# Kernel tuning notes

Measured on AMD Instinct MI355X. Metric: run time of the kernel, lower is better.

## Reference

```python
import jax, jax.numpy as jnp
import numpy as np

T = 1.0  # temperature from __init__ (t=1)


def setup_inputs() -> dict:
    key = jax.random.key(0)
    k1, k2, k3 = jax.random.split(key, 3)
    N, C, D = 262144, 1024, 128
    feats = jax.random.normal(k1, (N, D), dtype=jnp.float32)
    prototypes = jax.random.normal(k2, (C, D), dtype=jnp.float32)
    labels = jax.random.randint(k3, (N,), 0, C, dtype=jnp.int64)
    return {"feats": feats, "prototypes": prototypes, "labels": labels}


def _dce_loss(feats, prototypes, labels):
    # same math as sqrt(sum((x[:,None,:]-y)**2, -1)) without the NxCxD tensor.
    x_sq = jnp.sum(feats * feats, axis=-1, keepdims=True)          # [N,1]
    y_sq = jnp.sum(prototypes * prototypes, axis=-1)               # [C]
    xy = jnp.einsum('nd,cd->nc', feats, prototypes)                # [N,C]
    sq_dist = jnp.maximum(x_sq + y_sq[None, :] - 2.0 * xy, 0.0)
    logits = -jnp.sqrt(sq_dist) / T                                # [N,C]
    logp = jax.nn.log_softmax(logits, axis=-1)
    nll = -jnp.take_along_axis(logp, labels[:, None], axis=-1)[:, 0]
    return jnp.mean(nll)  # CrossEntropyLoss default reduction='mean'


def reference(feats, prototypes, labels):
    return _dce_loss(feats, prototypes, labels)
```

## Files before the change

kernel.cpp:

```cpp
#include <hip/hip_runtime.h>
#include <hip/hip_bf16.h>

typedef __bf16 bf16x8 __attribute__((ext_vector_type(8)));
typedef __bf16 bf16x2 __attribute__((ext_vector_type(2)));
typedef float f32x4 __attribute__((ext_vector_type(4)));

#define LN2f 0.6931471805599453f
#define CEf  2.0402785445f
#define EXPA (-CEf * 8388608.0f)
#define EXPB ((127.0f - 0.0437f) * 8388608.0f)

typedef __attribute__((address_space(3))) unsigned int lds_u32;
typedef __attribute__((address_space(1))) unsigned int glb_u32;

__device__ __forceinline__ void gload16(const void* g, void* l) {
    __builtin_amdgcn_global_load_lds((const glb_u32*)g, (lds_u32*)l, 16, 0, 0);
}

__global__ void dce_prep(const float* __restrict__ protos,
                         unsigned short* __restrict__ bpf,
                         float* __restrict__ ysqn) {
    int c = blockIdx.x;
    int lane = threadIdx.x;
    float2 f = ((const float2*)(protos))[c * 64 + lane];
    int d0 = lane * 2;
    int kk = d0 >> 5, sub = d0 & 31, lg = sub >> 3, e = sub & 7;
    size_t o = (((size_t)((c >> 4) * 4 + kk) * 64) + lg * 16 + (c & 15)) * 8 + e;
    bf16x2 h;
    h.x = (__bf16)f.x;
    h.y = (__bf16)f.y;
    *(bf16x2*)(bpf + o) = h;
    float xs = f.x * f.x + f.y * f.y;
#pragma unroll
    for (int d = 1; d < 64; d <<= 1) xs += __shfl_xor(xs, d);
    if (lane == 0) ysqn[c] = -0.5f * xs;
}

__global__ __launch_bounds__(256, 4) void dce_main(
    const float* __restrict__ feats,
    const float* __restrict__ protos,
    const unsigned short* __restrict__ bpf,
    const float* __restrict__ ysqn,
    const int* __restrict__ labels,
    float* __restrict__ partials, int C) {
    const int tid = threadIdx.x;
    const int lane = tid & 63;
    const int w = tid >> 6;
    const int row0 = blockIdx.x * 128;
    const int rbase = row0 + w * 32;
    const int lr = lane & 15;
    const int lg = lane >> 4;

    __shared__ __align__(16) unsigned char bsm0[16384];
    __shared__ __align__(16) unsigned char bsm1[16384];
    __shared__ float red[4];

    const char* bpc = (const char*)bpf;
    const int c0 = (blockIdx.x >> 3) & 15;

#define STAGE(buf, chunkIdx)                                                   \
    {                                                                          \
        const char* src_ = bpc + (size_t)(chunkIdx) * 16384 + tid * 16;        \
        _Pragma("unroll") for (int kt = 0; kt < 4; ++kt)                       \
            gload16(src_ + kt * 4096, (buf) + kt * 4096 + tid * 16);           \
    }

    STAGE(bsm0, c0);

    const int r1 = row0 + (tid >> 1);
    const int half = tid & 1;
    const int lab = labels[r1];
    const float4* fx = (const float4*)feats + (size_t)r1 * 32 + half * 16;
    const float4* px = (const float4*)protos + (size_t)lab * 32 + half * 16;
    float xx = 0.f, yy = 0.f, xy = 0.f;
#pragma unroll
    for (int i = 0; i < 16; ++i) {
        float4 f = fx[i], p = px[i];
        xx = fmaf(f.x, f.x, fmaf(f.y, f.y, fmaf(f.z, f.z, fmaf(f.w, f.w, xx))));
        yy = fmaf(p.x, p.x, fmaf(p.y, p.y, fmaf(p.z, p.z, fmaf(p.w, p.w, yy))));
        xy = fmaf(f.x, p.x, fmaf(f.y, p.y, fmaf(f.z, p.z, fmaf(f.w, p.w, xy))));
    }
    xx += __shfl_xor(xx, 1);
    yy += __shfl_xor(yy, 1);
    xy += __shfl_xor(xy, 1);
    const float ld = __builtin_amdgcn_sqrtf(fmaxf(fmaf(-2.f, xy, xx + yy), 0.f));

    bf16x8 a[2][4];
    const float4* f4 = (const float4*)feats;
#pragma unroll
    for (int m = 0; m < 2; ++m) {
        size_t r = (size_t)(rbase + m * 16 + lr);
#pragma unroll
        for (int kk = 0; kk < 4; ++kk) {
            size_t idx = r * 32 + kk * 8 + lg * 2;
            float4 lo = f4[idx];
            float4 hi = f4[idx + 1];
            bf16x8 v;
            v[0] = (__bf16)lo.x; v[1] = (__bf16)lo.y; v[2] = (__bf16)lo.z; v[3] = (__bf16)lo.w;
            v[4] = (__bf16)hi.x; v[5] = (__bf16)hi.y; v[6] = (__bf16)hi.z; v[7] = (__bf16)hi.w;
            a[m][kk] = v;
        }
    }

    float pre[2][4];
#pragma unroll
    for (int m = 0; m < 2; ++m)
#pragma unroll
        for (int reg = 0; reg < 4; ++reg)
            pre[m][reg] = -0.5f * __shfl(xx, 2 * (m * 16 + lg * 4 + reg));

    float lacc[2][4];
#pragma unroll
    for (int m = 0; m < 2; ++m)
#pragma unroll
        for (int reg = 0; reg < 4; ++reg) lacc[m][reg] = 0.f;

    const float* ysp = ysqn + lr;

#define TILE(buf, kt, tt)                                                       \
    {                                                                           \
        const bf16x8* bl_ = (const bf16x8*)((buf) + (kt) * 4096);               \
        bf16x8 b0 = bl_[lane];                                                  \
        bf16x8 b1 = bl_[64 + lane];                                             \
        bf16x8 b2 = bl_[128 + lane];                                            \
        bf16x8 b3 = bl_[192 + lane];                                            \
        const float yq_ = ysp[(tt) * 16];                                       \
        _Pragma("unroll") for (int m = 0; m < 2; ++m) {                         \
            f32x4 acc;                                                          \
            acc[0] = pre[m][0] + yq_;                                           \
            acc[1] = pre[m][1] + yq_;                                           \
            acc[2] = pre[m][2] + yq_;                                           \
            acc[3] = pre[m][3] + yq_;                                           \
            acc = __builtin_amdgcn_mfma_f32_16x16x32_bf16(a[m][0], b0, acc, 0, 0, 0); \
            acc = __builtin_amdgcn_mfma_f32_16x16x32_bf16(a[m][1], b1, acc, 0, 0, 0); \
            acc = __builtin_amdgcn_mfma_f32_16x16x32_bf16(a[m][2], b2, acc, 0, 0, 0); \
            acc = __builtin_amdgcn_mfma_f32_16x16x32_bf16(a[m][3], b3, acc, 0, 0, 0); \
            _Pragma("unroll") for (int reg = 0; reg < 4; ++reg) {               \
                float s_ = __builtin_amdgcn_sqrtf(-acc[reg]);  \
                int i_ = (int)fmaf(s_, EXPA, EXPB);            \
                lacc[m][reg] += __int_as_float(i_);                             \
            }                                                                   \
        }                                                                       \
    }

    __syncthreads();
#pragma unroll 2
    for (int ch = 0; ch < 16; ++ch) {
        unsigned char* curb = (ch & 1) ? bsm1 : bsm0;
        unsigned char* nxtb = (ch & 1) ? bsm0 : bsm1;
        const int ci = (c0 + ch) & 15;
        if (ch + 1 < 16) {
            const int ni = (c0 + ch + 1) & 15;
            STAGE(nxtb, ni);
        }
#pragma unroll
        for (int kt = 0; kt < 4; ++kt) TILE(curb, kt, ci * 4 + kt);
        __syncthreads();
    }

#undef STAGE
#undef TILE

    float ssum = 0.f;
#pragma unroll
    for (int m = 0; m < 2; ++m)
#pragma unroll
        for (int reg = 0; reg < 4; ++reg) {
            float l = lacc[m][reg];
            l += __shfl_xor(l, 1);
            l += __shfl_xor(l, 2);
            l += __shfl_xor(l, 4);
            l += __shfl_xor(l, 8);
            float ldv = __shfl(ld, 2 * (m * 16 + lg * 4 + reg));
            if (lr == 0) ssum += ldv + LN2f * __builtin_amdgcn_logf(l);
        }
    ssum += __shfl_xor(ssum, 16);
    ssum += __shfl_xor(ssum, 32);

    if (lane == 0) red[w] = ssum;
    __syncthreads();
    if (tid == 0) partials[blockIdx.x] = red[0] + red[1] + red[2] + red[3];
}

__global__ void dce_finish(const float* __restrict__ partials,
                           float* __restrict__ out, int nblocks, float invN) {
    int tid = threadIdx.x;
    float s = 0.f;
    for (int i = tid; i < nblocks; i += 256) s += partials[i];
#pragma unroll
    for (int d = 1; d < 64; d <<= 1) s += __shfl_xor(s, d);
    __shared__ float red[4];
    if ((tid & 63) == 0) red[tid >> 6] = s;
    __syncthreads();
    if (tid == 0) out[0] = (red[0] + red[1] + red[2] + red[3]) * invN;
}

extern "C" void kernel_launch(void* const* d_in, const int* in_sizes, int n_in,
                              void* d_out, int out_size, void* d_ws, size_t ws_size,
                              hipStream_t stream) {
    const float* feats = (const float*)d_in[0];
    const float* protos = (const float*)d_in[1];
    const int* labels = (const int*)d_in[2];
    const int N = in_sizes[2];
    const int C = in_sizes[1] / 128;
    float* out = (float*)d_out;

    unsigned short* bpf = (unsigned short*)d_ws;
    float* ysqn = (float*)((char*)d_ws + (size_t)C * 128 * 2);
    float* partials = ysqn + C;
    const int nblocks = N / 128;

    dce_prep<<<C, 64, 0, stream>>>(protos, bpf, ysqn);
    dce_main<<<nblocks, 256, 0, stream>>>(feats, protos, bpf, ysqn, labels, partials, C);
    dce_finish<<<1, 256, 0, stream>>>(partials, out, nblocks, 1.0f / (float)N);
}
```

Baseline: 130.4 us.

## Triple-buffer prototype tiles with partial vmcnt waits and stage ysq in LDS

Replaces the double-buffered LDS pipeline with a three-slot ring that prefetches two chunks ahead. It waits only on older loads (vmcnt(4)) before each barrier, so the next transfer stays in flight during compute. It also copies the per-prototype squared norms into LDS once instead of reading them from global memory per tile, and uses nontemporal loads for the streamed feature rows. The larger LDS footprint (about 52KB) forces launch bounds down to 3 blocks per CU, trading occupancy for deeper prefetch. The manual waitcnt and barrier logic also carries a correctness risk around buffer reuse.

Result: slower. 171.7 us (+31.6%).

```diff
diff --git a/kernel.cpp b/kernel.cpp
--- a/kernel.cpp
+++ b/kernel.cpp
@@ -36,7 +36,7 @@
     if (lane == 0) ysqn[c] = -0.5f * xs;
 }
 
-__global__ __launch_bounds__(256, 4) void dce_main(
+__global__ __launch_bounds__(256, 3) void dce_main(
     const float* __restrict__ feats,
     const float* __restrict__ protos,
     const unsigned short* __restrict__ bpf,
@@ -51,8 +51,8 @@
     const int lr = lane & 15;
     const int lg = lane >> 4;
 
-    __shared__ __align__(16) unsigned char bsm0[16384];
-    __shared__ __align__(16) unsigned char bsm1[16384];
+    __shared__ __align__(16) unsigned char bsm[3 * 16384];
+    __shared__ __align__(16) float ysql[1024];
     __shared__ float red[4];
 
     const char* bpc = (const char*)bpf;
@@ -65,20 +65,23 @@
             gload16(src_ + kt * 4096, (buf) + kt * 4096 + tid * 16);           \
     }
 
-    STAGE(bsm0, c0);
+    gload16((const char*)ysqn + tid * 16, (char*)ysql + tid * 16);
+    STAGE(bsm, c0);
+    STAGE(bsm + 16384, (c0 + 1) & 15);
 
     const int r1 = row0 + (tid >> 1);
     const int half = tid & 1;
     const int lab = labels[r1];
-    const float4* fx = (const float4*)feats + (size_t)r1 * 32 + half * 16;
-    const float4* px = (const float4*)protos + (size_t)lab * 32 + half * 16;
+    const f32x4* fx = (const f32x4*)(feats) + (size_t)r1 * 32 + half * 16;
+    const f32x4* px = (const f32x4*)(protos) + (size_t)lab * 32 + half * 16;
     float xx = 0.f, yy = 0.f, xy = 0.f;
 #pragma unroll
     for (int i = 0; i < 16; ++i) {
-        float4 f = fx[i], p = px[i];
-        xx = fmaf(f.x, f.x, fmaf(f.y, f.y, fmaf(f.z, f.z, fmaf(f.w, f.w, xx))));
-        yy = fmaf(p.x, p.x, fmaf(p.y, p.y, fmaf(p.z, p.z, fmaf(p.w, p.w, yy))));
-        xy = fmaf(f.x, p.x, fmaf(f.y, p.y, fmaf(f.z, p.z, fmaf(f.w, p.w, xy))));
+        f32x4 f = __builtin_nontemporal_load(fx + i);
+        f32x4 p = px[i];
+        xx = fmaf(f[0], f[0], fmaf(f[1], f[1], fmaf(f[2], f[2], fmaf(f[3], f[3], xx))));
+        yy = fmaf(p[0], p[0], fmaf(p[1], p[1], fmaf(p[2], p[2], fmaf(p[3], p[3], yy))));
+        xy = fmaf(f[0], p[0], fmaf(f[1], p[1], fmaf(f[2], p[2], fmaf(f[3], p[3], xy))));
     }
     xx += __shfl_xor(xx, 1);
     yy += __shfl_xor(yy, 1);
@@ -86,18 +89,18 @@
     const float ld = __builtin_amdgcn_sqrtf(fmaxf(fmaf(-2.f, xy, xx + yy), 0.f));
 
     bf16x8 a[2][4];
-    const float4* f4 = (const float4*)feats;
+    const f32x4* f4 = (const f32x4*)feats;
 #pragma unroll
     for (int m = 0; m < 2; ++m) {
         size_t r = (size_t)(rbase + m * 16 + lr);
 #pragma unroll
         for (int kk = 0; kk < 4; ++kk) {
             size_t idx = r * 32 + kk * 8 + lg * 2;
-            float4 lo = f4[idx];
-            float4 hi = f4[idx + 1];
+            f32x4 lo = __builtin_nontemporal_load(f4 + idx);
+            f32x4 hi = __builtin_nontemporal_load(f4 + idx + 1);
             bf16x8 v;
-            v[0] = (__bf16)lo.x; v[1] = (__bf16)lo.y; v[2] = (__bf16)lo.z; v[3] = (__bf16)lo.w;
-            v[4] = (__bf16)hi.x; v[5] = (__bf16)hi.y; v[6] = (__bf16)hi.z; v[7] = (__bf16)hi.w;
+            v[0] = (__bf16)lo[0]; v[1] = (__bf16)lo[1]; v[2] = (__bf16)lo[2]; v[3] = (__bf16)lo[3];
+            v[4] = (__bf16)hi[0]; v[5] = (__bf16)hi[1]; v[6] = (__bf16)hi[2]; v[7] = (__bf16)hi[3];
             a[m][kk] = v;
         }
     }
@@ -114,8 +117,6 @@
     for (int m = 0; m < 2; ++m)
 #pragma unroll
         for (int reg = 0; reg < 4; ++reg) lacc[m][reg] = 0.f;
-
-    const float* ysp = ysqn + lr;
 
 #define TILE(buf, kt, tt)                                                       \
     {                                                                           \
@@ -124,7 +125,7 @@
         bf16x8 b1 = bl_[64 + lane];                                             \
         bf16x8 b2 = bl_[128 + lane];                                            \
         bf16x8 b3 = bl_[192 + lane];                                            \
-        const float yq_ = ysp[(tt) * 16];                                       \
+        const float yq_ = ysql[(tt) * 16 + lr];                                 \
         _Pragma("unroll") for (int m = 0; m < 2; ++m) {                         \
             f32x4 acc;                                                          \
             acc[0] = pre[m][0] + yq_;                                           \
@@ -136,26 +137,35 @@
             acc = __builtin_amdgcn_mfma_f32_16x16x32_bf16(a[m][2], b2, acc, 0, 0, 0); \
             acc = __builtin_amdgcn_mfma_f32_16x16x32_bf16(a[m][3], b3, acc, 0, 0, 0); \
             _Pragma("unroll") for (int reg = 0; reg < 4; ++reg) {               \
-                float s_ = __builtin_amdgcn_sqrtf(-acc[reg]);  \
-                int i_ = (int)fmaf(s_, EXPA, EXPB);            \
+                float s_ = __builtin_amdgcn_sqrtf(-acc[reg]);                   \
+                int i_ = (int)fmaf(s_, EXPA, EXPB);                             \
                 lacc[m][reg] += __int_as_float(i_);                             \
             }                                                                   \
         }                                                                       \
     }
 
-    __syncthreads();
-#pragma unroll 2
+    asm volatile("s_waitcnt vmcnt(0)" ::: "memory");
+    __builtin_amdgcn_s_barrier();
+
+#pragma unroll 1
     for (int ch = 0; ch < 16; ++ch) {
-        unsigned char* curb = (ch & 1) ? bsm1 : bsm0;
-        unsigned char* nxtb = (ch & 1) ? bsm0 : bsm1;
+        unsigned char* curb = bsm + (ch % 3) * 16384;
         const int ci = (c0 + ch) & 15;
-        if (ch + 1 < 16) {
-            const int ni = (c0 + ch + 1) & 15;
-            STAGE(nxtb, ni);
-        }
-#pragma unroll
-        for (int kt = 0; kt < 4; ++kt) TILE(curb, kt, ci * 4 + kt);
-        __syncthreads();
+        if (ch < 14) {
+            unsigned char* nb = bsm + ((ch + 2) % 3) * 16384;
+            STAGE(nb, (ci + 2) & 15);
+        }
+        TILE(curb, 0, ci * 4 + 0);
+        TILE(curb, 1, ci * 4 + 1);
+        TILE(curb, 2, ci * 4 + 2);
+        TILE(curb, 3, ci * 4 + 3);
+        if (ch < 14) {
+            asm volatile("s_waitcnt vmcnt(4)" ::: "memory");
+            __builtin_amdgcn_s_barrier();
+        } else if (ch == 14) {
+            asm volatile("s_waitcnt vmcnt(0)" ::: "memory");
+            __builtin_amdgcn_s_barrier();
+        }
     }
 
 #undef STAGE
```
